# Optimization experiments

Measured on AMD Instinct MI355X. Metric: run time of the kernel, lower is better.

The kernel has to match this reference:

```python
import jax, jax.numpy as jnp
import numpy as np

N_PARENTS = 8
CHILDREN_PER_PARENT = 7
N_CHILDREN = N_PARENTS * CHILDREN_PER_PARENT  # 56 leaf classes
TOTAL_NODES = N_PARENTS + N_CHILDREN          # 64
BATCH = 262144


def _build_state_space():
    """Faithful port of generate_state_space for levels==2.

    Row 0 is the all-zero root state; then for each parent, one parent-only
    row, followed by one (parent, child) row per child. Shape [65, 64].
    """
    S = np.zeros((TOTAL_NODES + 1, TOTAL_NODES), dtype=np.float32)
    recorded = np.zeros(TOTAL_NODES)
    ii = 1
    for c in range(N_CHILDREN):
        p = N_CHILDREN + c // CHILDREN_PER_PARENT  # parent ids 56..63
        if recorded[p] == 0:
            S[ii, p] = 1.0
            recorded[p] = 1
            ii += 1
        S[ii, p] = 1.0
        S[ii, c] = 1.0
        ii += 1
    assert ii == TOTAL_NODES + 1, 'Invalid State Space'
    return jnp.asarray(S)


def setup_inputs() -> dict:
    key = jax.random.key(0)
    k1, k2 = jax.random.split(key)
    pred_label = jax.random.normal(k1, (BATCH, TOTAL_NODES), dtype=jnp.float32)
    gt_label = jax.random.randint(k2, (BATCH,), 0, N_CHILDREN, dtype=jnp.int32)
    return {
        'pred_label': pred_label,
        'gt_label': gt_label,
        'state_space': _build_state_space(),
    }


def reference(pred_label, gt_label, state_space):
    # index[s, b] = <state_space row s, pred_label[b]>  -> [S+1, B]
    index = state_space @ pred_label.T
    joint = jnp.exp(index)                      # [S+1, B]
    z = jnp.sum(joint, axis=0)                  # [B] partition function
    # Vectorized replacement of the per-sample Python loop:
    # rows of the state space that contain the ground-truth node.
    mask = state_space[:, gt_label] > 0         # [S+1, B]
    marginal = jnp.sum(jnp.where(mask, joint, jnp.zeros((), joint.dtype)), axis=0)  # [B]
    loss = -jnp.log(marginal / z)               # [B]
    return jnp.mean(loss)
```

## Files before the change

### kernel.cpp

```cpp
#include <hip/hip_runtime.h>


#define RPB     128
#define ROW_PAD 65
#define THREADS 256

__global__ void __launch_bounds__(THREADS) tree_loss_partial(
    const float* __restrict__ pred,
    const int*   __restrict__ gt,
    float*       __restrict__ partial,
    int rows)
{
    __shared__ float lds[RPB * ROW_PAD];
    __shared__ float zhalf[THREADS];
    __shared__ float wsum[THREADS / 64];

    const int t = threadIdx.x;
    const int rowBase = blockIdx.x * RPB;
    const bool full = (rowBase + RPB <= rows);

    const float4* p4 = (const float4*)pred + (size_t)rowBase * 16;
    #pragma unroll
    for (int i = 0; i < 8; ++i) {
        int f   = i * THREADS + t;
        int row = f >> 4;
        int col = (f & 15) << 2;
        if (full || rowBase + row < rows) {
            float4 v = p4[f];
            float* dst = &lds[row * ROW_PAD + col];
            dst[0] = __expf(v.x); dst[1] = __expf(v.y);
            dst[2] = __expf(v.z); dst[3] = __expf(v.w);
        }
    }
    __syncthreads();

    {
        const int r  = t & (RPB - 1);
        const int hi = t >> 7;
        float zh = 0.0f;
        if (full || rowBase + r < rows) {
            const float* e  = &lds[r * ROW_PAD];
            const float* ec = e + hi * 28;
            const float* ep = e + 56 + hi * 4;
            #pragma unroll
            for (int p = 0; p < 4; ++p) {
                float s = 1.0f;
                #pragma unroll
                for (int c = 0; c < 7; ++c) s += ec[p * 7 + c];
                zh += ep[p] * s;
            }
        }
        zhalf[t] = zh;
    }
    __syncthreads();

    float loss = 0.0f;
    if (t < RPB) {
        const int rowg = rowBase + t;
        if (rowg < rows) {
            float z = 1.0f + zhalf[t] + zhalf[t + RPB];
            const float* e = &lds[t * ROW_PAD];
            int g = gt[rowg];
            float m = e[g] * e[56 + g / 7];
            loss = __logf(z / m);
        }
    }

    #pragma unroll
    for (int off = 32; off; off >>= 1) loss += __shfl_xor(loss, off);
    if ((t & 63) == 0) wsum[t >> 6] = loss;
    __syncthreads();
    if (t == 0) {
        float b = 0.0f;
        #pragma unroll
        for (int w = 0; w < THREADS / 64; ++w) b += wsum[w];
        partial[blockIdx.x] = b;
    }
}

__global__ void __launch_bounds__(256) tree_loss_final(
    const float* __restrict__ partial, int n,
    float* __restrict__ out, float inv)
{
    float s = 0.0f;
    for (int i = threadIdx.x; i < n; i += 256) s += partial[i];
    #pragma unroll
    for (int off = 32; off; off >>= 1) s += __shfl_xor(s, off);
    __shared__ float w[4];
    const int lane = threadIdx.x & 63;
    const int wv   = threadIdx.x >> 6;
    if (lane == 0) w[wv] = s;
    __syncthreads();
    if (threadIdx.x == 0) out[0] = (w[0] + w[1] + w[2] + w[3]) * inv;
}

extern "C" void kernel_launch(void* const* d_in, const int* in_sizes, int n_in,
                              void* d_out, int out_size, void* d_ws, size_t ws_size,
                              hipStream_t stream) {
    const float* pred = (const float*)d_in[0];
    const int*   gt   = (const int*)d_in[1];
    float* out     = (float*)d_out;
    float* partial = (float*)d_ws;
    const int rows = in_sizes[1];

    const int blocks = (rows + RPB - 1) / RPB;
    tree_loss_partial<<<blocks, THREADS, 0, stream>>>(pred, gt, partial, rows);
    tree_loss_final<<<1, 256, 0, stream>>>(partial, blocks, out, 1.0f / (float)rows);
}
```

Baseline: 21.27 us.

## Compute one row per thread in registers instead of staging through LDS

Each thread now loads its full 64-float row with sixteen float4 loads, computes the exps and the partition function in registers, and drops the shared-memory staging and its two barriers. The marginal is computed in log space from the raw logits, re-read from global memory, which avoids two exps and a division. The cost is uncoalesced per-thread strided loads (256 bytes apart across lanes), higher register pressure, and fewer blocks from doubling the rows per block.

```diff
diff --git a/kernel.cpp b/kernel.cpp
--- a/kernel.cpp
+++ b/kernel.cpp
@@ -1,9 +1,12 @@
 #include <hip/hip_runtime.h>
 
 
-#define RPB     128
-#define ROW_PAD 65
+#define RPB     256
 #define THREADS 256
+
+__device__ __forceinline__ float elem(const float4& v, int j) {
+    return j == 0 ? v.x : j == 1 ? v.y : j == 2 ? v.z : v.w;
+}
 
 __global__ void __launch_bounds__(THREADS) tree_loss_partial(
     const float* __restrict__ pred,
@@ -11,59 +14,42 @@
     float*       __restrict__ partial,
     int rows)
 {
-    __shared__ float lds[RPB * ROW_PAD];
-    __shared__ float zhalf[THREADS];
     __shared__ float wsum[THREADS / 64];
 
-    const int t = threadIdx.x;
-    const int rowBase = blockIdx.x * RPB;
-    const bool full = (rowBase + RPB <= rows);
+    const int t   = threadIdx.x;
+    const int row = blockIdx.x * RPB + t;
 
-    const float4* p4 = (const float4*)pred + (size_t)rowBase * 16;
-    #pragma unroll
-    for (int i = 0; i < 8; ++i) {
-        int f   = i * THREADS + t;
-        int row = f >> 4;
-        int col = (f & 15) << 2;
-        if (full || rowBase + row < rows) {
-            float4 v = p4[f];
-            float* dst = &lds[row * ROW_PAD + col];
-            dst[0] = __expf(v.x); dst[1] = __expf(v.y);
-            dst[2] = __expf(v.z); dst[3] = __expf(v.w);
-        }
-    }
-    __syncthreads();
+    float loss = 0.0f;
+    if (row < rows) {
+        const float4* p4 = (const float4*)(pred + (size_t)row * 64);
 
-    {
-        const int r  = t & (RPB - 1);
-        const int hi = t >> 7;
-        float zh = 0.0f;
-        if (full || rowBase + r < rows) {
-            const float* e  = &lds[r * ROW_PAD];
-            const float* ec = e + hi * 28;
-            const float* ep = e + 56 + hi * 4;
+        float4 v[16];
+        #pragma unroll
+        for (int i = 0; i < 16; ++i) v[i] = p4[i];
+
+        float S[8];
+        #pragma unroll
+        for (int p = 0; p < 8; ++p) S[p] = 0.0f;
+        #pragma unroll
+        for (int i = 0; i < 14; ++i) {
             #pragma unroll
-            for (int p = 0; p < 4; ++p) {
-                float s = 1.0f;
-                #pragma unroll
-                for (int c = 0; c < 7; ++c) s += ec[p * 7 + c];
-                zh += ep[p] * s;
+            for (int j = 0; j < 4; ++j) {
+                constexpr int dummy = 0; (void)dummy;
+                const int col = 4 * i + j;
+                S[col / 7] += __expf(elem(v[i], j));
             }
         }
-        zhalf[t] = zh;
-    }
-    __syncthreads();
+        float z = 1.0f;
+        #pragma unroll
+        for (int p = 0; p < 8; ++p) {
+            const int i = (56 + p) >> 2, j = (56 + p) & 3;
+            z += __expf(elem(v[i], j)) * (1.0f + S[p]);
+        }
 
-    float loss = 0.0f;
-    if (t < RPB) {
-        const int rowg = rowBase + t;
-        if (rowg < rows) {
-            float z = 1.0f + zhalf[t] + zhalf[t + RPB];
-            const float* e = &lds[t * ROW_PAD];
-            int g = gt[rowg];
-            float m = e[g] * e[56 + g / 7];
-            loss = __logf(z / m);
-        }
+        int g = gt[row];
+        float xg = pred[(size_t)row * 64 + g];
+        float xp = pred[(size_t)row * 64 + 56 + g / 7];
+        loss = __logf(z) - xg - xp;
     }
 
     #pragma unroll
```

Result: slower. 24.56 us (+15.4%).
